# Kernel tuning notes

Measured on AMD Instinct MI355X. Metric: run time of the kernel, lower is better.

## Reference

```python
import jax, jax.numpy as jnp
from jax import lax
import numpy as np

B, L, D = 4, 4096, 1024
H = 16
HD = D // H          # 64
WIN = 256
NC = L // WIN
N_ITER = 50          # entmax-bisect iterations (entmax library default)
LN_EPS = 1e-5


def _p(x, am1):
    # clamp(x, min=0) ** (1/(alpha-1))
    return jnp.clip(x, 0.0) ** (1.0 / am1)


def entmax_bisect(X, alpha):
    """alpha-entmax along the last axis via bisection. alpha broadcastable to X."""
    am1 = alpha - 1.0
    Xs = X * am1
    d = X.shape[-1]
    max_val = Xs.max(axis=-1, keepdims=True)
    tau_lo = max_val - 1.0                       # 1 ** (alpha-1)
    tau_hi = max_val - (1.0 / d) ** am1
    f_lo = _p(Xs - tau_lo, am1).sum(-1, keepdims=True) - 1.0
    dm0 = tau_hi - tau_lo

    def body(i, carry):
        tau_lo, dm, _ = carry
        dm = dm * 0.5
        tau_m = tau_lo + dm
        f_m = _p(Xs - tau_m, am1).sum(-1, keepdims=True) - 1.0
        tau_lo = jnp.where(f_m * f_lo >= 0, tau_m, tau_lo)
        return (tau_lo, dm, tau_m)

    tau_lo, dm, tau_m = lax.fori_loop(0, N_ITER, body, (tau_lo, dm0, tau_lo))
    p = _p(Xs - tau_m, am1)
    return p / p.sum(-1, keepdims=True)          # ensure_sum_one


def setup_inputs() -> dict:
    key = jax.random.key(0)
    ks = jax.random.split(key, 4)
    x = jax.random.normal(ks[0], (B, L, D), jnp.float32)
    alpha = jnp.full((H,), 1.5, jnp.float32)
    qkv_w = 0.02 * jax.random.normal(ks[1], (3 * D, D), jnp.float32)
    qkv_b = jnp.zeros((3 * D,), jnp.float32)
    o_w = 0.02 * jax.random.normal(ks[2], (D, D), jnp.float32)
    o_b = jnp.zeros((D,), jnp.float32)
    ln_gamma = jnp.ones((D,), jnp.float32)
    ln_beta = jnp.zeros((D,), jnp.float32)
    return {"x": x, "alpha": alpha, "qkv_w": qkv_w, "qkv_b": qkv_b,
            "o_w": o_w, "o_b": o_b, "ln_gamma": ln_gamma, "ln_beta": ln_beta}


def reference(x, alpha, qkv_w, qkv_b, o_w, o_b, ln_gamma, ln_beta):
    # qkv projection -> [B, H, L, 3*HD]
    qkv = (x @ qkv_w.T + qkv_b).reshape(B, L, H, 3 * HD).transpose(0, 2, 1, 3)
    q, k, v = jnp.split(qkv, 3, axis=-1)
    # block-diagonal windows (span=None => k/v chunks coincide with q chunks)
    qc = q.reshape(B, H, NC, WIN, HD)
    kc = k.reshape(B, H, NC, WIN, HD)
    vc = v.reshape(B, H, NC, WIN, HD)
    scores = jnp.einsum('bhcqd,bhckd->bhcqk', qc, kc) / np.sqrt(HD).astype(np.float32)
    weights = entmax_bisect(scores, alpha.reshape(1, H, 1, 1, 1))
    out = jnp.einsum('bhcqk,bhckd->bhcqd', weights, vc)
    out = out.reshape(B, H, L, HD).transpose(0, 2, 1, 3).reshape(B, L, D)
    # layer norm
    mu = out.mean(-1, keepdims=True)
    var = out.var(-1, keepdims=True)
    out = (out - mu) * lax.rsqrt(var + LN_EPS) * ln_gamma + ln_beta
    return out @ o_w.T + o_b
```

## Files before the change

### kernel.cpp

```cpp
#include <hip/hip_runtime.h>

typedef unsigned short u16;
typedef unsigned int   u32;
typedef __attribute__((ext_vector_type(8))) short bf16x8;
typedef __attribute__((ext_vector_type(4))) float f32x4;
typedef __attribute__((ext_vector_type(8))) u16  u16x8;

__device__ __forceinline__ float b2f(u16 u) {
    union { u32 i; float f; } v; v.i = ((u32)u) << 16; return v.f;
}
__device__ __forceinline__ u16 f2b(float f) {
    u32 i = __float_as_uint(f);
    u32 r = (i + 0x7FFFu + ((i >> 16) & 1u)) >> 16;
    return (u16)r;
}
__device__ __forceinline__ bool is_bf16(const u32* gprobe) { return *gprobe == 0x3F803F80u; }

__device__ __forceinline__ void load_lds16(const void* g, void* l) {
    __builtin_amdgcn_global_load_lds((__attribute__((address_space(1))) void*)g,
                                     (__attribute__((address_space(3))) void*)l, 16, 0, 0);
}

__global__ __launch_bounds__(256) void cvt_kern(const void* __restrict__ src, u16* __restrict__ dst,
                                                int n8, const u32* __restrict__ gprobe) {
    const bool isb = is_bf16(gprobe);
    const int i = blockIdx.x * 256 + threadIdx.x;
    if (i >= n8) return;
    if (isb) {
        ((u16x8*)dst)[i] = ((const u16x8*)src)[i];
    } else {
        const float* s = (const float*)src + (size_t)i * 8;
        u16x8 o;
        #pragma unroll
        for (int j = 0; j < 8; j++) o[j] = f2b(s[j]);
        ((u16x8*)dst)[i] = o;
    }
}

__global__ __launch_bounds__(256) void gemm_bt(const u16* __restrict__ A, const u16* __restrict__ B,
                                               const void* __restrict__ bias,
                                               u16* __restrict__ Cb, float* __restrict__ Cf,
                                               const u32* __restrict__ gprobe, int out_mode,
                                               int M, int N, int K) {
    __shared__ u16 lsA[128 * 32];
    __shared__ u16 lsB[128 * 32];
    const int tid  = threadIdx.x;
    const int wave = tid >> 6, lane = tid & 63;
    const int m0 = blockIdx.y * 128, n0 = blockIdx.x * 128;
    const int wr = wave >> 1, wc = wave & 1;

    f32x4 acc[4][4] = {};

    const int srow = wave * 16 + (lane >> 2);
    const int scol = (lane & 3) * 8;
    const u16* gA0 = A + (size_t)(m0 + srow) * K + scol;
    const u16* gB0 = B + (size_t)(n0 + srow) * K + scol;
    u16* lA0 = &lsA[wave * 512];
    u16* lB0 = &lsB[wave * 512];
    const size_t rstep = (size_t)64 * K;

    for (int k0 = 0; k0 < K; k0 += 32) {
        __syncthreads();
        load_lds16(gA0 + k0,         lA0);
        load_lds16(gA0 + k0 + rstep, lA0 + 2048);
        load_lds16(gB0 + k0,         lB0);
        load_lds16(gB0 + k0 + rstep, lB0 + 2048);
        __syncthreads();

        bf16x8 af[4], bfr[4];
        #pragma unroll
        for (int mi = 0; mi < 4; mi++)
            af[mi] = *(const bf16x8*)&lsA[(wr * 64 + mi * 16 + (lane & 15)) * 32 + (lane >> 4) * 8];
        #pragma unroll
        for (int ni = 0; ni < 4; ni++)
            bfr[ni] = *(const bf16x8*)&lsB[(wc * 64 + ni * 16 + (lane & 15)) * 32 + (lane >> 4) * 8];
        #pragma unroll
        for (int mi = 0; mi < 4; mi++)
            #pragma unroll
            for (int ni = 0; ni < 4; ni++)
                acc[mi][ni] = __builtin_amdgcn_mfma_f32_16x16x32_bf16(af[mi], bfr[ni], acc[mi][ni], 0, 0, 0);
    }

    const bool isb     = is_bf16(gprobe);
    const bool store_b = (out_mode == 0) || isb;
    const int g = lane >> 4, cc = lane & 15;
    #pragma unroll
    for (int ni = 0; ni < 4; ni++) {
        const int col = n0 + wc * 64 + ni * 16 + cc;
        const float bv = isb ? b2f(((const u16*)bias)[col]) : ((const float*)bias)[col];
        #pragma unroll
        for (int mi = 0; mi < 4; mi++) {
            const int row = m0 + wr * 64 + mi * 16 + g * 4;
            #pragma unroll
            for (int i = 0; i < 4; i++) {
                const float v = acc[mi][ni][i] + bv;
                const size_t idx = (size_t)(row + i) * N + col;
                if (store_b) Cb[idx] = f2b(v);
                else         Cf[idx] = v;
            }
        }
    }
}

__device__ __forceinline__ void bfly_sum4(float (&a)[4]) {
    #pragma unroll
    for (int m = 1; m <= 8; m <<= 1)
        #pragma unroll
        for (int i = 0; i < 4; i++) a[i] += __shfl_xor(a[i], m, 64);
}

__device__ __forceinline__ void entmax2_rows(f32x4 (&s)[16], float inv_scl, float c2) {
    float mx[4] = {-3e38f, -3e38f, -3e38f, -3e38f};
    #pragma unroll
    for (int nt = 0; nt < 16; nt++)
        #pragma unroll
        for (int i = 0; i < 4; i++) mx[i] = fmaxf(mx[i], s[nt][i]);
    #pragma unroll
    for (int m = 1; m <= 8; m <<= 1)
        #pragma unroll
        for (int i = 0; i < 4; i++) mx[i] = fmaxf(mx[i], __shfl_xor(mx[i], m, 64));

    float tau[4];
    #pragma unroll
    for (int i = 0; i < 4; i++) tau[i] = mx[i] - inv_scl;

    #pragma unroll 1
    for (int it = 0; it < 10; it++) {
        float a2[4] = {0.f, 0.f, 0.f, 0.f};
        float a1[4] = {0.f, 0.f, 0.f, 0.f};
        #pragma unroll
        for (int nt = 0; nt < 16; nt++)
            #pragma unroll
            for (int i = 0; i < 4; i++) {
                float t = fmaxf(s[nt][i] - tau[i], 0.0f);
                a2[i] = fmaf(t, t, a2[i]);
                a1[i] += t;
            }
        bfly_sum4(a2);
        bfly_sum4(a1);
        #pragma unroll
        for (int i = 0; i < 4; i++)
            tau[i] += (a2[i] - c2) * 0.5f * __builtin_amdgcn_rcpf(a1[i]);
    }

    float ss[4] = {0.f, 0.f, 0.f, 0.f};
    #pragma unroll
    for (int nt = 0; nt < 16; nt++)
        #pragma unroll
        for (int i = 0; i < 4; i++) {
            float t = fmaxf(s[nt][i] - tau[i], 0.0f);
            float p = t * t;
            s[nt][i] = p;
            ss[i] += p;
        }
    bfly_sum4(ss);
    float inv[4];
    #pragma unroll
    for (int i = 0; i < 4; i++) inv[i] = 1.0f / ss[i];
    #pragma unroll
    for (int nt = 0; nt < 16; nt++)
        #pragma unroll
        for (int i = 0; i < 4; i++) s[nt][i] *= inv[i];
}

__device__ __forceinline__ void entmax_gen_rows(f32x4 (&s)[16], float e, float dm0) {
    float mx[4] = {-3e38f, -3e38f, -3e38f, -3e38f};
    #pragma unroll
    for (int nt = 0; nt < 16; nt++)
        #pragma unroll
        for (int i = 0; i < 4; i++) mx[i] = fmaxf(mx[i], s[nt][i]);
    #pragma unroll
    for (int m = 1; m <= 8; m <<= 1)
        #pragma unroll
        for (int i = 0; i < 4; i++) mx[i] = fmaxf(mx[i], __shfl_xor(mx[i], m, 64));

    float tau_lo[4], tau_m[4], f_lo[4];
    #pragma unroll
    for (int i = 0; i < 4; i++) { tau_lo[i] = mx[i] - 1.0f; tau_m[i] = tau_lo[i]; }
    {
        float a[4] = {0.f, 0.f, 0.f, 0.f};
        #pragma unroll
        for (int nt = 0; nt < 16; nt++)
            #pragma unroll
            for (int i = 0; i < 4; i++) {
                float t = fmaxf(s[nt][i] - tau_lo[i], 0.0f);
                a[i] += (t > 0.0f) ? __expf(e * __logf(t)) : 0.0f;
            }
        bfly_sum4(a);
        #pragma unroll
        for (int i = 0; i < 4; i++) f_lo[i] = a[i] - 1.0f;
    }
    float dm = dm0;
    #pragma unroll 1
    for (int it = 0; it < 26; it++) {
        dm *= 0.5f;
        #pragma unroll
        for (int i = 0; i < 4; i++) tau_m[i] = tau_lo[i] + dm;
        float a[4] = {0.f, 0.f, 0.f, 0.f};
        #pragma unroll
        for (int nt = 0; nt < 16; nt++)
            #pragma unroll
            for (int i = 0; i < 4; i++) {
                float t = fmaxf(s[nt][i] - tau_m[i], 0.0f);
                a[i] += (t > 0.0f) ? __expf(e * __logf(t)) : 0.0f;
            }
        bfly_sum4(a);
        #pragma unroll
        for (int i = 0; i < 4; i++)
            tau_lo[i] = ((a[i] - 1.0f) * f_lo[i] >= 0.0f) ? tau_m[i] : tau_lo[i];
    }
    float ss[4] = {0.f, 0.f, 0.f, 0.f};
    #pragma unroll
    for (int nt = 0; nt < 16; nt++)
        #pragma unroll
        for (int i = 0; i < 4; i++) {
            float t = fmaxf(s[nt][i] - tau_m[i], 0.0f);
            float p = (t > 0.0f) ? __expf(e * __logf(t)) : 0.0f;
            s[nt][i] = p;
            ss[i] += p;
        }
    bfly_sum4(ss);
    float inv[4];
    #pragma unroll
    for (int i = 0; i < 4; i++) inv[i] = 1.0f / ss[i];
    #pragma unroll
    for (int nt = 0; nt < 16; nt++)
        #pragma unroll
        for (int i = 0; i < 4; i++) s[nt][i] *= inv[i];
}

template<bool SQ>
__global__ __launch_bounds__(256, 2) void attn_win_t(const u16* __restrict__ qkv,
                                                     const void* __restrict__ alpha, u16* __restrict__ att,
                                                     const u32* __restrict__ gprobe) {
    __shared__ u16 Kl[256 * 64];
    __shared__ u16 Vt[64 * 256];
    __shared__ u16 Wl[4 * 16 * 64];
    const int tid  = threadIdx.x;
    const int wave = tid >> 6, lane = tid & 63;
    const int c = blockIdx.x, h = blockIdx.y, b = blockIdx.z;
    const int g = lane >> 4, cc = lane & 15;

    const float av  = is_bf16(gprobe) ? b2f(((const u16*)alpha)[h]) : ((const float*)alpha)[h];
    const float am1 = av - 1.0f;
    const float e   = 1.0f / am1;
    const bool  sq  = (e == 2.0f);
    if (SQ != sq) return;
    const float scl = am1 * 0.125f;
    const float inv_scl = 1.0f / scl;
    const float c2  = inv_scl * inv_scl;

    const size_t tok0 = (size_t)b * 4096 + (size_t)c * 256;
    const u16* qbase = qkv + tok0 * 3072 + h * 192;
    const u16* kbase = qbase + 64;
    const u16* vbase = qbase + 128;
    char* wl = (char*)&Wl[wave * (16 * 64)];

    {
        const int kr = tid >> 3, kc2 = tid & 7;
        #pragma unroll
        for (int it = 0; it < 8; it++) {
            const int row = it * 32 + kr;
            bf16x8 kv = *(const bf16x8*)(kbase + (size_t)row * 3072 + kc2 * 8);
            const int off = (row * 128 + kc2 * 16) ^ ((row & 7) << 4);
            *(bf16x8*)((char*)Kl + off) = kv;
        }
    }

    {
        const int d = tid & 63, tg = tid >> 6;
        #pragma unroll
        for (int j = 0; j < 8; j++) {
            const int t0 = tg * 64 + j * 8;
            u16x8 tmp;
            #pragma unroll
            for (int i = 0; i < 8; i++)
                tmp[i] = vbase[(size_t)(t0 + i) * 3072 + d];
            const int off = (d * 512 + t0 * 2) ^ ((d & 7) << 4);
            *(u16x8*)((char*)Vt + off) = tmp;
        }
    }
    __syncthreads();

    #pragma unroll 1
    for (int ch = 0; ch < 4; ch++) {
        const int r0 = ch * 64 + wave * 16;

        const u16* qr = qbase + (size_t)(r0 + cc) * 3072 + g * 8;
        bf16x8 q0 = *(const bf16x8*)qr;
        bf16x8 q1 = *(const bf16x8*)(qr + 32);

        f32x4 s[16] = {};
        #pragma unroll 4
        for (int nt = 0; nt < 16; nt++) {
            const int krow = nt * 16 + cc;
            const int swz  = (cc & 7) << 4;
            const int off0 = (krow * 128 + g * 16) ^ swz;
            const int off1 = (krow * 128 + g * 16 + 64) ^ swz;
            bf16x8 bk0 = *(const bf16x8*)((const char*)Kl + off0);
            bf16x8 bk1 = *(const bf16x8*)((const char*)Kl + off1);
            s[nt] = __builtin_amdgcn_mfma_f32_16x16x32_bf16(q0, bk0, s[nt], 0, 0, 0);
            s[nt] = __builtin_amdgcn_mfma_f32_16x16x32_bf16(q1, bk1, s[nt], 0, 0, 0);
        }

        if constexpr (SQ) {
            entmax2_rows(s, inv_scl, c2);
        } else {
            #pragma unroll
            for (int nt = 0; nt < 16; nt++)
                #pragma unroll
                for (int i = 0; i < 4; i++) s[nt][i] *= scl;
            const float dm0 = 1.0f - exp2f(-8.0f * am1);
            entmax_gen_rows(s, e, dm0);
        }

        f32x4 o[4] = {};
        #pragma unroll 2
        for (int kc = 0; kc < 8; kc++) {
            #pragma unroll
            for (int t = 0; t < 2; t++) {
                const int nt = kc * 2 + t;
                #pragma unroll
                for (int i = 0; i < 4; i++) {
                    const int wrow = g * 4 + i;
                    const int off  = (wrow * 128 + t * 32 + cc * 2) ^ ((wrow & 7) << 4);
                    *(u16*)(wl + off) = f2b(s[nt][i]);
                }
            }
            bf16x8 aw = *(const bf16x8*)(wl + ((cc * 128 + g * 16) ^ ((cc & 7) << 4)));
            #pragma unroll
            for (int nd = 0; nd < 4; nd++) {
                const int vrow = nd * 16 + cc;
                const int voff = (vrow * 512 + kc * 64 + g * 16) ^ ((cc & 7) << 4);
                bf16x8 bv = *(const bf16x8*)((const char*)Vt + voff);
                o[nd] = __builtin_amdgcn_mfma_f32_16x16x32_bf16(aw, bv, o[nd], 0, 0, 0);
            }
        }

        #pragma unroll
        for (int nd = 0; nd < 4; nd++)
            #pragma unroll
            for (int i = 0; i < 4; i++) {
                const int wrow = g * 4 + i;
                const int off  = (wrow * 128 + nd * 32 + cc * 2) ^ ((wrow & 7) << 4);
                *(u16*)(wl + off) = f2b(o[nd][i]);
            }
        #pragma unroll
        for (int p = 0; p < 2; p++) {
            const int row = p * 8 + (lane >> 3);
            const int off = (row * 128 + (lane & 7) * 16) ^ ((row & 7) << 4);
            u16x8 val = *(const u16x8*)(wl + off);
            *(u16x8*)(att + (size_t)(tok0 + r0 + row) * 1024 + h * 64 + (lane & 7) * 8) = val;
        }
    }
}

__global__ __launch_bounds__(256) void ln_kern(const u16* __restrict__ att, const void* __restrict__ gam,
                                               const void* __restrict__ bet, u16* __restrict__ out,
                                               const u32* __restrict__ gprobe) {
    const bool isb = is_bf16(gprobe);
    const int tid = threadIdx.x;
    const int wave = tid >> 6, lane = tid & 63;
    const size_t tok = (size_t)blockIdx.x * 4 + wave;
    const u16* p = att + tok * 1024 + lane * 16;
    u16x8 v0 = *(const u16x8*)p;
    u16x8 v1 = *(const u16x8*)(p + 8);
    float x[16];
    #pragma unroll
    for (int j = 0; j < 8; j++) { x[j] = b2f(v0[j]); x[j + 8] = b2f(v1[j]); }
    float s = 0.f, s2 = 0.f;
    #pragma unroll
    for (int j = 0; j < 16; j++) { s += x[j]; s2 = fmaf(x[j], x[j], s2); }
    #pragma unroll
    for (int m = 1; m <= 32; m <<= 1) { s += __shfl_xor(s, m, 64); s2 += __shfl_xor(s2, m, 64); }
    const float mean = s * (1.0f / 1024.0f);
    const float var  = s2 * (1.0f / 1024.0f) - mean * mean;
    const float rs   = rsqrtf(var + 1e-5f);

    float gv[16], bv[16];
    if (isb) {
        const u16* gp = (const u16*)gam + lane * 16;
        const u16* bp = (const u16*)bet + lane * 16;
        u16x8 g0 = *(const u16x8*)gp, g1 = *(const u16x8*)(gp + 8);
        u16x8 b0 = *(const u16x8*)bp, b1 = *(const u16x8*)(bp + 8);
        #pragma unroll
        for (int j = 0; j < 8; j++) {
            gv[j] = b2f(g0[j]); gv[j + 8] = b2f(g1[j]);
            bv[j] = b2f(b0[j]); bv[j + 8] = b2f(b1[j]);
        }
    } else {
        const float* gp = (const float*)gam + lane * 16;
        const float* bp = (const float*)bet + lane * 16;
        #pragma unroll
        for (int j = 0; j < 16; j++) { gv[j] = gp[j]; bv[j] = bp[j]; }
    }

    u16x8 w0, w1;
    #pragma unroll
    for (int j = 0; j < 8; j++) {
        w0[j] = f2b((x[j]     - mean) * rs * gv[j]     + bv[j]);
        w1[j] = f2b((x[j + 8] - mean) * rs * gv[j + 8] + bv[j + 8]);
    }
    u16* op = out + tok * 1024 + lane * 16;
    *(u16x8*)op       = w0;
    *(u16x8*)(op + 8) = w1;
}

extern "C" void kernel_launch(void* const* d_in, const int* in_sizes, int n_in,
                              void* d_out, int out_size, void* d_ws, size_t ws_size,
                              hipStream_t stream) {
    const void* x      = d_in[0];
    const void* alpha  = d_in[1];
    const void* qkv_w  = d_in[2];
    const void* qkv_b  = d_in[3];
    const void* o_w    = d_in[4];
    const void* o_b    = d_in[5];
    const u32*  gprobe = (const u32*)d_in[6];
    const void* gam    = d_in[6];
    const void* bet    = d_in[7];

    u16* xb  = (u16*)d_ws;
    u16* wq  = xb + (size_t)16384 * 1024;
    u16* wo  = wq + (size_t)3072 * 1024;
    u16* qkv = wo + (size_t)1024 * 1024;
    u16* att = (u16*)d_out;
    u16* ln  = xb;

    dim3 blk(256);
    cvt_kern<<<dim3((16384 * 1024 / 8 + 255) / 256), blk, 0, stream>>>(x, xb, 16384 * 1024 / 8, gprobe);
    cvt_kern<<<dim3((3072 * 1024 / 8 + 255) / 256), blk, 0, stream>>>(qkv_w, wq, 3072 * 1024 / 8, gprobe);
    cvt_kern<<<dim3((1024 * 1024 / 8 + 255) / 256), blk, 0, stream>>>(o_w, wo, 1024 * 1024 / 8, gprobe);
    gemm_bt<<<dim3(3072 / 128, 16384 / 128), blk, 0, stream>>>(xb, wq, qkv_b, qkv, nullptr, gprobe, 0,
                                                               16384, 3072, 1024);
    attn_win_t<true ><<<dim3(16, 16, 4), blk, 0, stream>>>(qkv, alpha, att, gprobe);
    attn_win_t<false><<<dim3(16, 16, 4), blk, 0, stream>>>(qkv, alpha, att, gprobe);
    ln_kern<<<dim3(4096), blk, 0, stream>>>(att, gam, bet, ln, gprobe);
    gemm_bt<<<dim3(1024 / 128, 16384 / 128), blk, 0, stream>>>(ln, wo, o_b, (u16*)d_out, (float*)d_out,
                                                               gprobe, 1, 16384, 1024, 1024);
}
```

Measured before the change: 600.5 us.

## Transpose QK^T MFMA output so each lane holds one query row

Swaps the MFMA operands so the score tile is transposed and each lane's accumulator values belong to a single query row. Per-row reductions in the entmax loops then need only a local sum plus two cross-lane shuffles, not four shuffles per each of four rows, and tau becomes a scalar per lane. The probability write to LDS becomes one packed 4x16-bit store per tile instead of four scalar stores. The cost is a change in the LDS write layout, which must still match the later weight read.

```diff
diff --git a/kernel.cpp b/kernel.cpp
--- a/kernel.cpp
+++ b/kernel.cpp
@@ -5,6 +5,7 @@
 typedef __attribute__((ext_vector_type(8))) short bf16x8;
 typedef __attribute__((ext_vector_type(4))) float f32x4;
 typedef __attribute__((ext_vector_type(8))) u16  u16x8;
+typedef __attribute__((ext_vector_type(4))) u16  u16x4;
 
 __device__ __forceinline__ float b2f(u16 u) {
     union { u32 i; float f; } v; v.i = ((u32)u) << 16; return v.f;
@@ -102,131 +103,120 @@
     }
 }
 
-__device__ __forceinline__ void bfly_sum4(float (&a)[4]) {
-    #pragma unroll
-    for (int m = 1; m <= 8; m <<= 1)
-        #pragma unroll
-        for (int i = 0; i < 4; i++) a[i] += __shfl_xor(a[i], m, 64);
-}
-
-__device__ __forceinline__ void entmax2_rows(f32x4 (&s)[16], float inv_scl, float c2) {
+__device__ __forceinline__ void entmax2_rowsT(f32x4 (&s)[16], float inv_scl, float c2) {
     float mx[4] = {-3e38f, -3e38f, -3e38f, -3e38f};
     #pragma unroll
     for (int nt = 0; nt < 16; nt++)
         #pragma unroll
         for (int i = 0; i < 4; i++) mx[i] = fmaxf(mx[i], s[nt][i]);
-    #pragma unroll
-    for (int m = 1; m <= 8; m <<= 1)
-        #pragma unroll
-        for (int i = 0; i < 4; i++) mx[i] = fmaxf(mx[i], __shfl_xor(mx[i], m, 64));
-
-    float tau[4];
-    #pragma unroll
-    for (int i = 0; i < 4; i++) tau[i] = mx[i] - inv_scl;
+    float m = fmaxf(fmaxf(mx[0], mx[1]), fmaxf(mx[2], mx[3]));
+    m = fmaxf(m, __shfl_xor(m, 16, 64));
+    m = fmaxf(m, __shfl_xor(m, 32, 64));
+
+    float tau = m - inv_scl;
 
     #pragma unroll 1
     for (int it = 0; it < 10; it++) {
-        float a2[4] = {0.f, 0.f, 0.f, 0.f};
-        float a1[4] = {0.f, 0.f, 0.f, 0.f};
+        float p2[4] = {0.f, 0.f, 0.f, 0.f};
+        float p1[4] = {0.f, 0.f, 0.f, 0.f};
         #pragma unroll
         for (int nt = 0; nt < 16; nt++)
             #pragma unroll
             for (int i = 0; i < 4; i++) {
-                float t = fmaxf(s[nt][i] - tau[i], 0.0f);
-                a2[i] = fmaf(t, t, a2[i]);
-                a1[i] += t;
-            }
-        bfly_sum4(a2);
-        bfly_sum4(a1);
-        #pragma unroll
-        for (int i = 0; i < 4; i++)
-            tau[i] += (a2[i] - c2) * 0.5f * __builtin_amdgcn_rcpf(a1[i]);
-    }
-
-    float ss[4] = {0.f, 0.f, 0.f, 0.f};
+                float t = fmaxf(s[nt][i] - tau, 0.0f);
+                p2[i] = fmaf(t, t, p2[i]);
+                p1[i] += t;
+            }
+        float a2 = (p2[0] + p2[1]) + (p2[2] + p2[3]);
+        float a1 = (p1[0] + p1[1]) + (p1[2] + p1[3]);
+        a2 += __shfl_xor(a2, 16, 64);
+        a2 += __shfl_xor(a2, 32, 64);
+        a1 += __shfl_xor(a1, 16, 64);
+        a1 += __shfl_xor(a1, 32, 64);
+        tau += (a2 - c2) * 0.5f * __builtin_amdgcn_rcpf(a1);
+    }
+
+    float sp[4] = {0.f, 0.f, 0.f, 0.f};
     #pragma unroll
     for (int nt = 0; nt < 16; nt++)
         #pragma unroll
         for (int i = 0; i < 4; i++) {
-            float t = fmaxf(s[nt][i] - tau[i], 0.0f);
+            float t = fmaxf(s[nt][i] - tau, 0.0f);
             float p = t * t;
             s[nt][i] = p;
-            ss[i] += p;
-        }
-    bfly_sum4(ss);
-    float inv[4];
-    #pragma unroll
-    for (int i = 0; i < 4; i++) inv[i] = 1.0f / ss[i];
-    #pragma unroll
-    for (int nt = 0; nt < 16; nt++)
-        #pragma unroll
-        for (int i = 0; i < 4; i++) s[nt][i] *= inv[i];
-}
-
-__device__ __forceinline__ void entmax_gen_rows(f32x4 (&s)[16], float e, float dm0) {
+            sp[i] += p;
+        }
+    float ss = (sp[0] + sp[1]) + (sp[2] + sp[3]);
+    ss += __shfl_xor(ss, 16, 64);
+    ss += __shfl_xor(ss, 32, 64);
+    const float inv = 1.0f / ss;
+    #pragma unroll
+    for (int nt = 0; nt < 16; nt++)
+        #pragma unroll
+        for (int i = 0; i < 4; i++) s[nt][i] *= inv;
+}
+
+__device__ __forceinline__ void entmax_gen_rowsT(f32x4 (&s)[16], float e, float dm0) {
     float mx[4] = {-3e38f, -3e38f, -3e38f, -3e38f};
     #pragma unroll
     for (int nt = 0; nt < 16; nt++)
         #pragma unroll
         for (int i = 0; i < 4; i++) mx[i] = fmaxf(mx[i], s[nt][i]);
-    #pragma unroll
-    for (int m = 1; m <= 8; m <<= 1)
-        #pragma unroll
-        for (int i = 0; i < 4; i++) mx[i] = fmaxf(mx[i], __shfl_xor(mx[i], m, 64));
-
-    float tau_lo[4], tau_m[4], f_lo[4];
-    #pragma unroll
-    for (int i = 0; i < 4; i++) { tau_lo[i] = mx[i] - 1.0f; tau_m[i] = tau_lo[i]; }
+    float m = fmaxf(fmaxf(mx[0], mx[1]), fmaxf(mx[2], mx[3]));
+    m = fmaxf(m, __shfl_xor(m, 16, 64));
+    m = fmaxf(m, __shfl_xor(m, 32, 64));
+
+    float tau_lo = m - 1.0f, tau_m = tau_lo, f_lo;
     {
-        float a[4] = {0.f, 0.f, 0.f, 0.f};
+        float p[4] = {0.f, 0.f, 0.f, 0.f};
         #pragma unroll
         for (int nt = 0; nt < 16; nt++)
             #pragma unroll
             for (int i = 0; i < 4; i++) {
-                float t = fmaxf(s[nt][i] - tau_lo[i], 0.0f);
-                a[i] += (t > 0.0f) ? __expf(e * __logf(t)) : 0.0f;
-            }
-        bfly_sum4(a);
-        #pragma unroll
-        for (int i = 0; i < 4; i++) f_lo[i] = a[i] - 1.0f;
+                float t = fmaxf(s[nt][i] - tau_lo, 0.0f);
+                p[i] += (t > 0.0f) ? __expf(e * __logf(t)) : 0.0f;
+            }
+        float a = (p[0] + p[1]) + (p[2] + p[3]);
+        a += __shfl_xor(a, 16, 64);
+        a += __shfl_xor(a, 32, 64);
+        f_lo = a - 1.0f;
     }
     float dm = dm0;
     #pragma unroll 1
     for (int it = 0; it < 26; it++) {
         dm *= 0.5f;
-        #pragma unroll
-        for (int i = 0; i < 4; i++) tau_m[i] = tau_lo[i] + dm;
-        float a[4] = {0.f, 0.f, 0.f, 0.f};
+        tau_m = tau_lo + dm;
+        float p[4] = {0.f, 0.f, 0.f, 0.f};
         #pragma unroll
         for (int nt = 0; nt < 16; nt++)
             #pragma unroll
             for (int i = 0; i < 4; i++) {
-                float t = fmaxf(s[nt][i] - tau_m[i], 0.0f);
-                a[i] += (t > 0.0f) ? __expf(e * __logf(t)) : 0.0f;
-            }
-        bfly_sum4(a);
-        #pragma unroll
-        for (int i = 0; i < 4; i++)
-            tau_lo[i] = ((a[i] - 1.0f) * f_lo[i] >= 0.0f) ? tau_m[i] : tau_lo[i];
-    }
-    float ss[4] = {0.f, 0.f, 0.f, 0.f};
+                float t = fmaxf(s[nt][i] - tau_m, 0.0f);
+                p[i] += (t > 0.0f) ? __expf(e * __logf(t)) : 0.0f;
+            }
+        float a = (p[0] + p[1]) + (p[2] + p[3]);
+        a += __shfl_xor(a, 16, 64);
+        a += __shfl_xor(a, 32, 64);
+        if ((a - 1.0f) * f_lo >= 0.0f) tau_lo = tau_m;
+    }
+    float sp[4] = {0.f, 0.f, 0.f, 0.f};
     #pragma unroll
     for (int nt = 0; nt < 16; nt++)
         #pragma unroll
         for (int i = 0; i < 4; i++) {
-            float t = fmaxf(s[nt][i] - tau_m[i], 0.0f);
+            float t = fmaxf(s[nt][i] - tau_m, 0.0f);
             float p = (t > 0.0f) ? __expf(e * __logf(t)) : 0.0f;
             s[nt][i] = p;
-            ss[i] += p;
-        }
-    bfly_sum4(ss);
-    float inv[4];
-    #pragma unroll
-    for (int i = 0; i < 4; i++) inv[i] = 1.0f / ss[i];
-    #pragma unroll
-    for (int nt = 0; nt < 16; nt++)
-        #pragma unroll
-        for (int i = 0; i < 4; i++) s[nt][i] *= inv[i];
+            sp[i] += p;
+        }
+    float ss = (sp[0] + sp[1]) + (sp[2] + sp[3]);
+    ss += __shfl_xor(ss, 16, 64);
+    ss += __shfl_xor(ss, 32, 64);
+    const float inv = 1.0f / ss;
+    #pragma unroll
+    for (int nt = 0; nt < 16; nt++)
+        #pragma unroll
+        for (int i = 0; i < 4; i++) s[nt][i] *= inv;
 }
 
 template<bool SQ>
@@ -299,19 +289,19 @@
             const int off1 = (krow * 128 + g * 16 + 64) ^ swz;
             bf16x8 bk0 = *(const bf16x8*)((const char*)Kl + off0);
             bf16x8 bk1 = *(const bf16x8*)((const char*)Kl + off1);
-            s[nt] = __builtin_amdgcn_mfma_f32_16x16x32_bf16(q0, bk0, s[nt], 0, 0, 0);
-            s[nt] = __builtin_amdgcn_mfma_f32_16x16x32_bf16(q1, bk1, s[nt], 0, 0, 0);
+            s[nt] = __builtin_amdgcn_mfma_f32_16x16x32_bf16(bk0, q0, s[nt], 0, 0, 0);
+            s[nt] = __builtin_amdgcn_mfma_f32_16x16x32_bf16(bk1, q1, s[nt], 0, 0, 0);
         }
 
         if constexpr (SQ) {
-            entmax2_rows(s, inv_scl, c2);
+            entmax2_rowsT(s, inv_scl, c2);
         } else {
             #pragma unroll
             for (int nt = 0; nt < 16; nt++)
                 #pragma unroll
                 for (int i = 0; i < 4; i++) s[nt][i] *= scl;
             const float dm0 = 1.0f - exp2f(-8.0f * am1);
-            entmax_gen_rows(s, e, dm0);
+            entmax_gen_rowsT(s, e, dm0);
         }
 
         f32x4 o[4] = {};
@@ -320,12 +310,11 @@
             #pragma unroll
             for (int t = 0; t < 2; t++) {
                 const int nt = kc * 2 + t;
+                u16x4 pk;
                 #pragma unroll
-                for (int i = 0; i < 4; i++) {
-                    const int wrow = g * 4 + i;
-                    const int off  = (wrow * 128 + t * 32 + cc * 2) ^ ((wrow & 7) << 4);
-                    *(u16*)(wl + off) = f2b(s[nt][i]);
-                }
+                for (int i = 0; i < 4; i++) pk[i] = f2b(s[nt][i]);
+                const int off = (cc * 128 + t * 32 + g * 8) ^ ((cc & 7) << 4);
+                *(u16x4*)(wl + off) = pk;
             }
             bf16x8 aw = *(const bf16x8*)(wl + ((cc * 128 + g * 16) ^ ((cc & 7) << 4)));
             #pragma unroll
```

Result: faster. 580.6 us (-3.3%).
